# Performance work log

Hardware: AMD Instinct MI355X
Metric: run time of the kernel (lower is better)

The kernel has to match this reference:

```python
import jax, jax.numpy as jnp
import numpy as np

FEAT_DIM = 256
NUM_HEADS = 8
HEAD_DIM = FEAT_DIM // NUM_HEADS
N_NODES = 4096
LN_EPS = 1e-5


def setup_inputs() -> dict:
    key = jax.random.key(0)
    ks = jax.random.split(key, 10)
    C = FEAT_DIM
    s = 1.0 / np.sqrt(C)
    x = jax.random.normal(ks[0], (N_NODES, C), dtype=jnp.float32)
    Wq = jax.random.uniform(ks[1], (C, C), jnp.float32, -s, s)
    bq = jax.random.uniform(ks[2], (C,), jnp.float32, -s, s)
    Wk = jax.random.uniform(ks[3], (C, C), jnp.float32, -s, s)
    bk = jax.random.uniform(ks[4], (C,), jnp.float32, -s, s)
    Wv = jax.random.uniform(ks[5], (C, C), jnp.float32, -s, s)
    bv = jax.random.uniform(ks[6], (C,), jnp.float32, -s, s)
    Wo = jax.random.uniform(ks[7], (C, C), jnp.float32, -s, s)
    bo = jax.random.uniform(ks[8], (C,), jnp.float32, -s, s)
    scale = jnp.float32(1.0 / np.sqrt(HEAD_DIM))
    gamma = jnp.ones((C,), jnp.float32)
    beta = jnp.zeros((C,), jnp.float32)
    return {"x": x, "Wq": Wq, "bq": bq, "Wk": Wk, "bk": bk, "Wv": Wv,
            "bv": bv, "scale": scale, "Wo": Wo, "bo": bo,
            "gamma": gamma, "beta": beta}


def reference(x, Wq, bq, Wk, bk, Wv, bv, scale, Wo, bo, gamma, beta):
    N, C = x.shape
    H, D = NUM_HEADS, HEAD_DIM
    q = (x @ Wq + bq).reshape(N, H, D)
    k = (x @ Wk + bk).reshape(N, H, D)
    v = (x @ Wv + bv).reshape(N, H, D)
    # scores[i, j, h]; softmax over j (the key/node axis), per original dim=1
    scores = jnp.einsum('ihd,jhd->ijh', q, k) * scale
    attn = jax.nn.softmax(scores, axis=1)
    messages = jnp.einsum('ijh,jhd->ihd', attn, v).reshape(N, H * D)
    y = x + messages @ Wo + bo
    # LayerNorm over last dim
    mu = jnp.mean(y, axis=-1, keepdims=True)
    var = jnp.mean(jnp.square(y - mu), axis=-1, keepdims=True)
    return (y - mu) * jax.lax.rsqrt(var + LN_EPS) * gamma + beta
```

## Files before the change

kernel.cpp:

```cpp
#include <hip/hip_runtime.h>
#include <hip/hip_bf16.h>
#include <math.h>

#define NN 4096
#define C  256
#define NH 8
#define HD 32
#define LN_EPS 1e-5f
#define LOG2E 1.44269504088896340736f

typedef unsigned short u16;
typedef __attribute__((ext_vector_type(8))) short bf16x8;
typedef __attribute__((ext_vector_type(4))) float f32x4;

__device__ inline u16 f2b(float f) {
    union { float f; unsigned u; } v; v.f = f;
    unsigned r = (v.u + 0x7fff + ((v.u >> 16) & 1)) >> 16;
    return (u16)r;
}

__device__ inline void atomic_add_agent(float* p, float v) {
    __hip_atomic_fetch_add(p, v, __ATOMIC_RELAXED, __HIP_MEMORY_SCOPE_AGENT);
}

__global__ __launch_bounds__(256) void transpose_w_kernel(
    const float* __restrict__ Wq, const float* __restrict__ Wk,
    const float* __restrict__ Wv, const float* __restrict__ Wo,
    u16* __restrict__ WqkvT, u16* __restrict__ WoT)
{
    __shared__ float tile[32][33];
    const int z = blockIdx.z;
    const float* W = (z == 0) ? Wq : (z == 1) ? Wk : (z == 2) ? Wv : Wo;
    u16* WT = (z == 3) ? WoT : (WqkvT + (size_t)z * 256 * 256);
    const int tx = threadIdx.x & 31, ty = threadIdx.x >> 5;
    const int n0 = blockIdx.x * 32, k0 = blockIdx.y * 32;
    #pragma unroll
    for (int i = 0; i < 32; i += 8)
        tile[ty + i][tx] = W[(size_t)(k0 + ty + i) * 256 + n0 + tx];
    __syncthreads();
    #pragma unroll
    for (int i = 0; i < 32; i += 8)
        WT[(size_t)(n0 + ty + i) * 256 + k0 + tx] = f2b(tile[tx][ty + i]);
}

__global__ __launch_bounds__(256) void qkv_mfma_kernel(
    const float* __restrict__ x, const u16* __restrict__ WT,
    const float* __restrict__ bq, const float* __restrict__ bk,
    const float* __restrict__ bv, const float* __restrict__ scale_p,
    u16* __restrict__ qb, u16* __restrict__ kb, u16* __restrict__ vT)
{
    const int m0 = blockIdx.x * 64;
    const int n0 = blockIdx.y * 64;
    const int t = threadIdx.x;
    const int wave = t >> 6, lane = t & 63;
    const int l16 = lane & 15, quad = lane >> 4;

    f32x4 acc[4];
    #pragma unroll
    for (int ct = 0; ct < 4; ++ct) acc[ct] = f32x4{0.f, 0.f, 0.f, 0.f};

    const float* xrow = x + (size_t)(m0 + wave * 16 + l16) * C;
    #pragma unroll
    for (int kk = 0; kk < 8; ++kk) {
        const float4 a0 = *(const float4*)(xrow + kk * 32 + quad * 8);
        const float4 a1 = *(const float4*)(xrow + kk * 32 + quad * 8 + 4);
        union { __hip_bfloat162 h2[4]; bf16x8 v; } af;
        af.h2[0] = __float22bfloat162_rn(float2{a0.x, a0.y});
        af.h2[1] = __float22bfloat162_rn(float2{a0.z, a0.w});
        af.h2[2] = __float22bfloat162_rn(float2{a1.x, a1.y});
        af.h2[3] = __float22bfloat162_rn(float2{a1.z, a1.w});
        #pragma unroll
        for (int ct = 0; ct < 4; ++ct) {
            const bf16x8 bfr = *(const bf16x8*)(
                WT + (size_t)(n0 + ct * 16 + l16) * C + kk * 32 + quad * 8);
            acc[ct] = __builtin_amdgcn_mfma_f32_16x16x32_bf16(af.v, bfr, acc[ct], 0, 0, 0);
        }
    }

    const int sect = n0 >> 8;
    const int c0 = n0 & 255;
    const int rbase = m0 + wave * 16 + quad * 4;
    if (sect == 0) {
        const float scl = (*scale_p) * LOG2E;
        #pragma unroll
        for (int ct = 0; ct < 4; ++ct) {
            const int c = c0 + ct * 16 + l16;
            const float b = bq[c];
            #pragma unroll
            for (int r = 0; r < 4; ++r)
                qb[(size_t)(rbase + r) * C + c] = f2b((acc[ct][r] + b) * scl);
        }
    } else if (sect == 1) {
        #pragma unroll
        for (int ct = 0; ct < 4; ++ct) {
            const int c = c0 + ct * 16 + l16;
            const float b = bk[c];
            #pragma unroll
            for (int r = 0; r < 4; ++r)
                kb[(size_t)(rbase + r) * C + c] = f2b(acc[ct][r] + b);
        }
    } else {
        #pragma unroll
        for (int ct = 0; ct < 4; ++ct) {
            const int c = c0 + ct * 16 + l16;
            const float b = bv[c];
            union { u16 u[4]; unsigned long long ull; } pk;
            #pragma unroll
            for (int r = 0; r < 4; ++r) pk.u[r] = f2b(acc[ct][r] + b);
            *(unsigned long long*)(vT + (size_t)c * NN + rbase) = pk.ull;
        }
    }
}

#define TQ 64
#define TJ 64
#define NZ 4
#define ZT (NN / NZ)
#define KSTRIDE 40
#define VSTRIDE 72

__global__ __launch_bounds__(256) void attn_mfma_kernel(
    const u16* __restrict__ q, const u16* __restrict__ k,
    const u16* __restrict__ vT, float* __restrict__ msgacc,
    float* __restrict__ lacc)
{
    __shared__ u16 Ks[TJ * KSTRIDE];
    __shared__ u16 Vs[HD * VSTRIDE];
    __shared__ u16 Ps[4][16 * VSTRIDE];

    const int qbase = blockIdx.x * TQ;
    const int h = blockIdx.y;
    const int z = blockIdx.z;
    const int t = threadIdx.x;
    const int wave = t >> 6;
    const int lane = t & 63;
    const int l16 = lane & 15;
    const int quad = lane >> 4;

    const bf16x8 qfrag = *(const bf16x8*)(
        q + (size_t)(qbase + wave * 16 + l16) * C + h * HD + quad * 8);

    float lsum = 0.f;
    f32x4 o0 = {0.f, 0.f, 0.f, 0.f};
    f32x4 o1 = {0.f, 0.f, 0.f, 0.f};

    const int sj = t >> 2, sc = t & 3;
    const int sd = t >> 3, se = t & 7;

    for (int j0 = z * ZT; j0 < z * ZT + ZT; j0 += TJ) {
        __syncthreads();
        *(bf16x8*)(Ks + sj * KSTRIDE + sc * 8) =
            *(const bf16x8*)(k + (size_t)(j0 + sj) * C + h * HD + sc * 8);
        *(bf16x8*)(Vs + sd * VSTRIDE + se * 8) =
            *(const bf16x8*)(vT + (size_t)(h * HD + sd) * NN + j0 + se * 8);
        __syncthreads();

        f32x4 st[4];
        #pragma unroll
        for (int ct = 0; ct < 4; ++ct) {
            const bf16x8 kf = *(const bf16x8*)(Ks + (ct * 16 + l16) * KSTRIDE + quad * 8);
            f32x4 zz = {0.f, 0.f, 0.f, 0.f};
            st[ct] = __builtin_amdgcn_mfma_f32_16x16x32_bf16(kf, qfrag, zz, 0, 0, 0);
        }

        #pragma unroll
        for (int ct = 0; ct < 4; ++ct) {
            const float e0 = exp2f(st[ct][0]);
            const float e1 = exp2f(st[ct][1]);
            const float e2 = exp2f(st[ct][2]);
            const float e3 = exp2f(st[ct][3]);
            lsum += (e0 + e1) + (e2 + e3);
            union { __hip_bfloat162 h2[2]; unsigned long long ull; } pk;
            pk.h2[0] = __float22bfloat162_rn(float2{e0, e1});
            pk.h2[1] = __float22bfloat162_rn(float2{e2, e3});
            *(unsigned long long*)(&Ps[wave][l16 * VSTRIDE + ct * 16 + quad * 4]) = pk.ull;
        }

        asm volatile("s_waitcnt lgkmcnt(0)" ::: "memory");

        #pragma unroll
        for (int ks = 0; ks < 2; ++ks) {
            const bf16x8 pf = *(const bf16x8*)(&Ps[wave][l16 * VSTRIDE + ks * 32 + quad * 8]);
            const bf16x8 vf0 = *(const bf16x8*)(Vs + l16 * VSTRIDE + ks * 32 + quad * 8);
            const bf16x8 vf1 = *(const bf16x8*)(Vs + (16 + l16) * VSTRIDE + ks * 32 + quad * 8);
            o0 = __builtin_amdgcn_mfma_f32_16x16x32_bf16(pf, vf0, o0, 0, 0, 0);
            o1 = __builtin_amdgcn_mfma_f32_16x16x32_bf16(pf, vf1, o1, 0, 0, 0);
        }
    }

    lsum += __shfl_xor(lsum, 16);
    lsum += __shfl_xor(lsum, 32);
    if (quad == 0)
        atomic_add_agent(&lacc[(size_t)(qbase + wave * 16 + l16) * NH + h], lsum);

    #pragma unroll
    for (int r = 0; r < 4; ++r) {
        const int row = qbase + wave * 16 + quad * 4 + r;
        atomic_add_agent(&msgacc[(size_t)row * C + h * HD + l16], o0[r]);
        atomic_add_agent(&msgacc[(size_t)row * C + h * HD + 16 + l16], o1[r]);
    }
}

__global__ __launch_bounds__(256) void out_ln_mfma_kernel(
    const float* __restrict__ msgacc, const float* __restrict__ lacc,
    const u16* __restrict__ WoT, const float* __restrict__ bo,
    const float* __restrict__ x, const float* __restrict__ gamma,
    const float* __restrict__ beta, float* __restrict__ out)
{
    __shared__ float sums[2][4][16];
    const int m0 = blockIdx.x * 16;
    const int t = threadIdx.x;
    const int w = t >> 6, lane = t & 63;
    const int l16 = lane & 15, quad = lane >> 4;

    f32x4 acc[4];
    #pragma unroll
    for (int ct = 0; ct < 4; ++ct) acc[ct] = f32x4{0.f, 0.f, 0.f, 0.f};

    const float* arow = msgacc + (size_t)(m0 + l16) * C;
    const float* lrow = lacc + (size_t)(m0 + l16) * NH;
    #pragma unroll
    for (int kk = 0; kk < 8; ++kk) {
        const float li = 1.f / lrow[kk];
        const float4 a0 = *(const float4*)(arow + kk * 32 + quad * 8);
        const float4 a1 = *(const float4*)(arow + kk * 32 + quad * 8 + 4);
        union { __hip_bfloat162 h2[4]; bf16x8 v; } af;
        af.h2[0] = __float22bfloat162_rn(float2{a0.x * li, a0.y * li});
        af.h2[1] = __float22bfloat162_rn(float2{a0.z * li, a0.w * li});
        af.h2[2] = __float22bfloat162_rn(float2{a1.x * li, a1.y * li});
        af.h2[3] = __float22bfloat162_rn(float2{a1.z * li, a1.w * li});
        #pragma unroll
        for (int ct = 0; ct < 4; ++ct) {
            const bf16x8 bfr = *(const bf16x8*)(
                WoT + (size_t)(w * 64 + ct * 16 + l16) * C + kk * 32 + quad * 8);
            acc[ct] = __builtin_amdgcn_mfma_f32_16x16x32_bf16(af.v, bfr, acc[ct], 0, 0, 0);
        }
    }

    float val[4][4];
    #pragma unroll
    for (int r = 0; r < 4; ++r) {
        const int row = m0 + quad * 4 + r;
        float sr = 0.f, qr = 0.f;
        #pragma unroll
        for (int ct = 0; ct < 4; ++ct) {
            const int c = w * 64 + ct * 16 + l16;
            const float v = acc[ct][r] + bo[c] + x[(size_t)row * C + c];
            val[ct][r] = v;
            sr += v;
            qr = fmaf(v, v, qr);
        }
        sr += __shfl_xor(sr, 1); sr += __shfl_xor(sr, 2);
        sr += __shfl_xor(sr, 4); sr += __shfl_xor(sr, 8);
        qr += __shfl_xor(qr, 1); qr += __shfl_xor(qr, 2);
        qr += __shfl_xor(qr, 4); qr += __shfl_xor(qr, 8);
        if (l16 == 0) {
            sums[0][w][quad * 4 + r] = sr;
            sums[1][w][quad * 4 + r] = qr;
        }
    }
    __syncthreads();

    #pragma unroll
    for (int r = 0; r < 4; ++r) {
        const int ri = quad * 4 + r;
        const int row = m0 + ri;
        const float tot  = sums[0][0][ri] + sums[0][1][ri] + sums[0][2][ri] + sums[0][3][ri];
        const float tot2 = sums[1][0][ri] + sums[1][1][ri] + sums[1][2][ri] + sums[1][3][ri];
        const float mu = tot * (1.f / C);
        const float var = fmaxf(tot2 * (1.f / C) - mu * mu, 0.f);
        const float rstd = rsqrtf(var + LN_EPS);
        #pragma unroll
        for (int ct = 0; ct < 4; ++ct) {
            const int c = w * 64 + ct * 16 + l16;
            out[(size_t)row * C + c] = (val[ct][r] - mu) * rstd * gamma[c] + beta[c];
        }
    }
}

extern "C" void kernel_launch(void* const* d_in, const int* in_sizes, int n_in,
                              void* d_out, int out_size, void* d_ws, size_t ws_size,
                              hipStream_t stream) {
    const float* x     = (const float*)d_in[0];
    const float* Wq    = (const float*)d_in[1];
    const float* bq    = (const float*)d_in[2];
    const float* Wk    = (const float*)d_in[3];
    const float* bk    = (const float*)d_in[4];
    const float* Wv    = (const float*)d_in[5];
    const float* bv    = (const float*)d_in[6];
    const float* scale = (const float*)d_in[7];
    const float* Wo    = (const float*)d_in[8];
    const float* bo    = (const float*)d_in[9];
    const float* gamma = (const float*)d_in[10];
    const float* beta  = (const float*)d_in[11];
    float* out = (float*)d_out;

    u16* qb     = (u16*)d_ws;
    u16* kb     = qb + (size_t)NN * C;
    u16* vT     = kb + (size_t)NN * C;
    u16* WqkvT  = vT + (size_t)NN * C;
    u16* WoT    = WqkvT + (size_t)3 * C * C;
    float* msgacc = (float*)(WoT + (size_t)C * C);
    float* lacc   = msgacc + (size_t)NN * C;

    hipMemsetAsync(msgacc, 0, (size_t)NN * C * sizeof(float), stream);
    hipMemsetAsync(lacc, 0, (size_t)NN * NH * sizeof(float), stream);

    transpose_w_kernel<<<dim3(8, 8, 4), 256, 0, stream>>>(Wq, Wk, Wv, Wo,
                                                          WqkvT, WoT);
    qkv_mfma_kernel<<<dim3(NN / 64, 12), 256, 0, stream>>>(
        x, WqkvT, bq, bk, bv, scale, qb, kb, vT);
    attn_mfma_kernel<<<dim3(NN / TQ, NH, NZ), 256, 0, stream>>>(
        qb, kb, vT, msgacc, lacc);
    out_ln_mfma_kernel<<<NN / 16, 256, 0, stream>>>(msgacc, lacc, WoT, bo, x,
                                                    gamma, beta, out);
}
```

Measured before the change: 176.4 us.

## Pre-convert x to bf16, merge memsets, halve rows per out_ln block

Adds a kernel that converts x to bf16 once, so the QKV GEMM no longer re-reads fp32 x and converts it in each of its 12 column blocks. The two memsets become one contiguous memset. The output/LayerNorm kernel now handles 8 rows per block instead of 16, doubling the block count for more parallelism, though half of each MFMA tile is computed and then thrown away. The trade-off is one extra kernel launch and an extra bf16 copy of x in workspace.

Result: faster. 169.7 us (-3.8%).

```diff
diff --git a/kernel.cpp b/kernel.cpp
--- a/kernel.cpp
+++ b/kernel.cpp
@@ -23,6 +23,17 @@
     __hip_atomic_fetch_add(p, v, __ATOMIC_RELAXED, __HIP_MEMORY_SCOPE_AGENT);
 }
 
+__global__ __launch_bounds__(256) void xconv_kernel(
+    const float* __restrict__ x, u16* __restrict__ xb)
+{
+    const int i = (blockIdx.x * 256 + threadIdx.x) * 4;
+    const float4 v = *(const float4*)(x + i);
+    union { u16 u[4]; unsigned long long ull; } pk;
+    pk.u[0] = f2b(v.x); pk.u[1] = f2b(v.y);
+    pk.u[2] = f2b(v.z); pk.u[3] = f2b(v.w);
+    *(unsigned long long*)(xb + i) = pk.ull;
+}
+
 __global__ __launch_bounds__(256) void transpose_w_kernel(
     const float* __restrict__ Wq, const float* __restrict__ Wk,
     const float* __restrict__ Wv, const float* __restrict__ Wo,
@@ -44,7 +55,7 @@
 }
 
 __global__ __launch_bounds__(256) void qkv_mfma_kernel(
-    const float* __restrict__ x, const u16* __restrict__ WT,
+    const u16* __restrict__ xb, const u16* __restrict__ WT,
     const float* __restrict__ bq, const float* __restrict__ bk,
     const float* __restrict__ bv, const float* __restrict__ scale_p,
     u16* __restrict__ qb, u16* __restrict__ kb, u16* __restrict__ vT)
@@ -59,21 +70,15 @@
     #pragma unroll
     for (int ct = 0; ct < 4; ++ct) acc[ct] = f32x4{0.f, 0.f, 0.f, 0.f};
 
-    const float* xrow = x + (size_t)(m0 + wave * 16 + l16) * C;
+    const u16* xrow = xb + (size_t)(m0 + wave * 16 + l16) * C;
     #pragma unroll
     for (int kk = 0; kk < 8; ++kk) {
-        const float4 a0 = *(const float4*)(xrow + kk * 32 + quad * 8);
-        const float4 a1 = *(const float4*)(xrow + kk * 32 + quad * 8 + 4);
-        union { __hip_bfloat162 h2[4]; bf16x8 v; } af;
-        af.h2[0] = __float22bfloat162_rn(float2{a0.x, a0.y});
-        af.h2[1] = __float22bfloat162_rn(float2{a0.z, a0.w});
-        af.h2[2] = __float22bfloat162_rn(float2{a1.x, a1.y});
-        af.h2[3] = __float22bfloat162_rn(float2{a1.z, a1.w});
+        const bf16x8 af = *(const bf16x8*)(xrow + kk * 32 + quad * 8);
         #pragma unroll
         for (int ct = 0; ct < 4; ++ct) {
             const bf16x8 bfr = *(const bf16x8*)(
                 WT + (size_t)(n0 + ct * 16 + l16) * C + kk * 32 + quad * 8);
-            acc[ct] = __builtin_amdgcn_mfma_f32_16x16x32_bf16(af.v, bfr, acc[ct], 0, 0, 0);
+            acc[ct] = __builtin_amdgcn_mfma_f32_16x16x32_bf16(af, bfr, acc[ct], 0, 0, 0);
         }
     }
 
@@ -201,14 +206,15 @@
     }
 }
 
+#define OROWS 8
 __global__ __launch_bounds__(256) void out_ln_mfma_kernel(
     const float* __restrict__ msgacc, const float* __restrict__ lacc,
     const u16* __restrict__ WoT, const float* __restrict__ bo,
     const float* __restrict__ x, const float* __restrict__ gamma,
     const float* __restrict__ beta, float* __restrict__ out)
 {
-    __shared__ float sums[2][4][16];
-    const int m0 = blockIdx.x * 16;
+    __shared__ float sums[2][4][OROWS];
+    const int m0 = blockIdx.x * OROWS;
     const int t = threadIdx.x;
     const int w = t >> 6, lane = t & 63;
     const int l16 = lane & 15, quad = lane >> 4;
@@ -217,8 +223,9 @@
     #pragma unroll
     for (int ct = 0; ct < 4; ++ct) acc[ct] = f32x4{0.f, 0.f, 0.f, 0.f};
 
-    const float* arow = msgacc + (size_t)(m0 + l16) * C;
-    const float* lrow = lacc + (size_t)(m0 + l16) * NH;
+    const int ar = min(m0 + l16, NN - 1);
+    const float* arow = msgacc + (size_t)ar * C;
+    const float* lrow = lacc + (size_t)ar * NH;
     #pragma unroll
     for (int kk = 0; kk < 8; ++kk) {
         const float li = 1.f / lrow[kk];
@@ -238,42 +245,46 @@
     }
 
     float val[4][4];
-    #pragma unroll
-    for (int r = 0; r < 4; ++r) {
-        const int row = m0 + quad * 4 + r;
-        float sr = 0.f, qr = 0.f;
-        #pragma unroll
-        for (int ct = 0; ct < 4; ++ct) {
-            const int c = w * 64 + ct * 16 + l16;
-            const float v = acc[ct][r] + bo[c] + x[(size_t)row * C + c];
-            val[ct][r] = v;
-            sr += v;
-            qr = fmaf(v, v, qr);
-        }
-        sr += __shfl_xor(sr, 1); sr += __shfl_xor(sr, 2);
-        sr += __shfl_xor(sr, 4); sr += __shfl_xor(sr, 8);
-        qr += __shfl_xor(qr, 1); qr += __shfl_xor(qr, 2);
-        qr += __shfl_xor(qr, 4); qr += __shfl_xor(qr, 8);
-        if (l16 == 0) {
-            sums[0][w][quad * 4 + r] = sr;
-            sums[1][w][quad * 4 + r] = qr;
+    if (quad < 2) {
+        #pragma unroll
+        for (int r = 0; r < 4; ++r) {
+            const int row = m0 + quad * 4 + r;
+            float sr = 0.f, qr = 0.f;
+            #pragma unroll
+            for (int ct = 0; ct < 4; ++ct) {
+                const int c = w * 64 + ct * 16 + l16;
+                const float v = acc[ct][r] + bo[c] + x[(size_t)row * C + c];
+                val[ct][r] = v;
+                sr += v;
+                qr = fmaf(v, v, qr);
+            }
+            sr += __shfl_xor(sr, 1); sr += __shfl_xor(sr, 2);
+            sr += __shfl_xor(sr, 4); sr += __shfl_xor(sr, 8);
+            qr += __shfl_xor(qr, 1); qr += __shfl_xor(qr, 2);
+            qr += __shfl_xor(qr, 4); qr += __shfl_xor(qr, 8);
+            if (l16 == 0) {
+                sums[0][w][quad * 4 + r] = sr;
+                sums[1][w][quad * 4 + r] = qr;
+            }
         }
     }
     __syncthreads();
 
-    #pragma unroll
-    for (int r = 0; r < 4; ++r) {
-        const int ri = quad * 4 + r;
-        const int row = m0 + ri;
-        const float tot  = sums[0][0][ri] + sums[0][1][ri] + sums[0][2][ri] + sums[0][3][ri];
-        const float tot2 = sums[1][0][ri] + sums[1][1][ri] + sums[1][2][ri] + sums[1][3][ri];
-        const float mu = tot * (1.f / C);
-        const float var = fmaxf(tot2 * (1.f / C) - mu * mu, 0.f);
-        const float rstd = rsqrtf(var + LN_EPS);
-        #pragma unroll
-        for (int ct = 0; ct < 4; ++ct) {
-            const int c = w * 64 + ct * 16 + l16;
-            out[(size_t)row * C + c] = (val[ct][r] - mu) * rstd * gamma[c] + beta[c];
+    if (quad < 2) {
+        #pragma unroll
+        for (int r = 0; r < 4; ++r) {
+            const int ri = quad * 4 + r;
+            const int row = m0 + ri;
+            const float tot  = sums[0][0][ri] + sums[0][1][ri] + sums[0][2][ri] + sums[0][3][ri];
+            const float tot2 = sums[1][0][ri] + sums[1][1][ri] + sums[1][2][ri] + sums[1][3][ri];
+            const float mu = tot * (1.f / C);
+            const float var = fmaxf(tot2 * (1.f / C) - mu * mu, 0.f);
+            const float rstd = rsqrtf(var + LN_EPS);
+            #pragma unroll
+            for (int ct = 0; ct < 4; ++ct) {
+                const int c = w * 64 + ct * 16 + l16;
+                out[(size_t)row * C + c] = (val[ct][r] - mu) * rstd * gamma[c] + beta[c];
+            }
         }
     }
 }
@@ -298,20 +309,22 @@
     u16* qb     = (u16*)d_ws;
     u16* kb     = qb + (size_t)NN * C;
     u16* vT     = kb + (size_t)NN * C;
-    u16* WqkvT  = vT + (size_t)NN * C;
+    u16* xbuf   = vT + (size_t)NN * C;
+    u16* WqkvT  = xbuf + (size_t)NN * C;
     u16* WoT    = WqkvT + (size_t)3 * C * C;
     float* msgacc = (float*)(WoT + (size_t)C * C);
     float* lacc   = msgacc + (size_t)NN * C;
 
-    hipMemsetAsync(msgacc, 0, (size_t)NN * C * sizeof(float), stream);
-    hipMemsetAsync(lacc, 0, (size_t)NN * NH * sizeof(float), stream);
-
+    hipMemsetAsync(msgacc, 0, ((size_t)NN * C + (size_t)NN * NH) * sizeof(float),
+                   stream);
+
+    xconv_kernel<<<NN * C / (256 * 4), 256, 0, stream>>>(x, xbuf);
     transpose_w_kernel<<<dim3(8, 8, 4), 256, 0, stream>>>(Wq, Wk, Wv, Wo,
                                                           WqkvT, WoT);
     qkv_mfma_kernel<<<dim3(NN / 64, 12), 256, 0, stream>>>(
-        x, WqkvT, bq, bk, bv, scale, qb, kb, vT);
+        xbuf, WqkvT, bq, bk, bv, scale, qb, kb, vT);
     attn_mfma_kernel<<<dim3(NN / TQ, NH, NZ), 256, 0, stream>>>(
         qb, kb, vT, msgacc, lacc);
-    out_ln_mfma_kernel<<<NN / 16, 256, 0, stream>>>(msgacc, lacc, WoT, bo, x,
-                                                    gamma, beta, out);
-}
+    out_ln_mfma_kernel<<<NN / OROWS, 256, 0, stream>>>(msgacc, lacc, WoT, bo, x,
+                                                       gamma, beta, out);
+}
```
